# Kernel optimization log

Hardware: AMD Instinct MI355X
Metric: run time of the kernel (lower is better)

The kernel has to match this reference:

```python
import jax, jax.numpy as jnp
import numpy as np

_LAYER_SHAPES = ((10, 8), (8, 8), (8, 1))


def setup_inputs() -> dict:
    key = jax.random.key(0)
    k1, k2, k3, k4 = jax.random.split(key, 4)
    B, D, H, W = 8, 8, 256, 256
    M = 256
    E = jax.random.normal(k1, (B, D, H, W), dtype=jnp.float32)
    theta = jax.random.normal(k2, (M, 169), dtype=jnp.float32)
    centers = jax.random.uniform(k3, (M, 2), dtype=jnp.float32)
    batch_index = jax.random.randint(k4, (M,), 0, B)
    return {"E": E, "theta": theta, "centers": centers, "batch_index": batch_index}


def reference(E, theta, centers, batch_index):
    B, D, H, W = E.shape
    M = theta.shape[0]
    dt = E.dtype
    # pixel-center grid in [0,1]: linspace(0.5/H, 1-0.5/H, H)
    ys = (jnp.arange(H, dtype=dt) + 0.5) / H
    xs = (jnp.arange(W, dtype=dt) + 0.5) / W
    grid_y, grid_x = jnp.meshgrid(ys, xs, indexing="ij")
    grid = jnp.stack([grid_x, grid_y], axis=0)  # (2, H, W), channel order (x, y)
    rel = grid[None] - centers.astype(dt)[:, :, None, None]  # (M, 2, H, W)

    e_per_match = E[batch_index]  # (M, D, H, W) gather
    x = jnp.concatenate([e_per_match, rel], axis=1)  # (M, D+2, H, W)

    # split flat theta into per-layer 1x1 conv weights/biases and apply
    offset = 0
    n_layers = len(_LAYER_SHAPES)
    for li, (c_in, c_out) in enumerate(_LAYER_SHAPES):
        w = theta[:, offset:offset + c_in * c_out].reshape(M, c_out, c_in)
        offset += c_in * c_out
        b = theta[:, offset:offset + c_out]
        offset += c_out
        # per-instance 1x1 conv == tiny batched matmul over channels
        x = jnp.einsum("moi,mihw->mohw", w, x) + b[:, :, None, None]
        if li < n_layers - 1:
            x = jax.nn.gelu(x, approximate=False)  # torch F.gelu default (erf)
    return x[:, 0]  # (M, H, W) mask logits
```

## Files before the change

### kernel.cpp

```cpp
#include <hip/hip_runtime.h>
#include <math.h>

#define HWPIX 65536
#define NMATCH 256
#define THETA_LEN 169

__device__ __forceinline__ float gelu_fast(float v) {
    float t = fmaf(v * v, 0.10294323f, 2.3022082f);
    float e = __builtin_amdgcn_exp2f(-v * t);
    float r = __builtin_amdgcn_rcpf(1.0f + e);
    return v * r;
}

__global__ __launch_bounds__(256) void dmh_kernel(
    const float* __restrict__ E,
    const float* __restrict__ theta,
    const float* __restrict__ centers,
    const int*   __restrict__ bidx,
    float* __restrict__ out)
{
    const int m    = blockIdx.x >> 6;
    const int tile = blockIdx.x & 63;
    const int p0   = tile * 1024 + threadIdx.x * 4;

    const float* __restrict__ th = theta + m * THETA_LEN;
    const float cx = centers[2 * m];
    const float cy = centers[2 * m + 1];
    const int   b  = bidx[m];
    const float* __restrict__ Eb = E + (size_t)b * (8 * HWPIX) + p0;

    const int h = p0 >> 8;
    const int w = p0 & 255;

    float x[10][4];
    #pragma unroll
    for (int c = 0; c < 8; ++c) {
        const float4 v = *(const float4*)(Eb + (size_t)c * HWPIX);
        x[c][0] = v.x; x[c][1] = v.y; x[c][2] = v.z; x[c][3] = v.w;
    }
    #pragma unroll
    for (int j = 0; j < 4; ++j) {
        x[8][j] = (w + j + 0.5f) * (1.0f / 256.0f) - cx;
        x[9][j] = (h + 0.5f) * (1.0f / 256.0f) - cy;
    }

    float y[8][4];
    #pragma unroll
    for (int o = 0; o < 8; ++o) {
        const float bias = th[80 + o];
        float a[4] = {bias, bias, bias, bias};
        #pragma unroll
        for (int i = 0; i < 10; ++i) {
            const float wv = th[o * 10 + i];
            #pragma unroll
            for (int j = 0; j < 4; ++j) a[j] = fmaf(wv, x[i][j], a[j]);
        }
        #pragma unroll
        for (int j = 0; j < 4; ++j) y[o][j] = gelu_fast(a[j]);
    }

    float z[8][4];
    #pragma unroll
    for (int o = 0; o < 8; ++o) {
        const float bias = th[152 + o];
        float a[4] = {bias, bias, bias, bias};
        #pragma unroll
        for (int i = 0; i < 8; ++i) {
            const float wv = th[88 + o * 8 + i];
            #pragma unroll
            for (int j = 0; j < 4; ++j) a[j] = fmaf(wv, y[i][j], a[j]);
        }
        #pragma unroll
        for (int j = 0; j < 4; ++j) z[o][j] = gelu_fast(a[j]);
    }

    const float b2 = th[168];
    float r[4] = {b2, b2, b2, b2};
    #pragma unroll
    for (int i = 0; i < 8; ++i) {
        const float wv = th[160 + i];
        #pragma unroll
        for (int j = 0; j < 4; ++j) r[j] = fmaf(wv, z[i][j], r[j]);
    }

    float4 o4;
    o4.x = r[0]; o4.y = r[1]; o4.z = r[2]; o4.w = r[3];
    *(float4*)(out + (size_t)m * HWPIX + p0) = o4;
}

extern "C" void kernel_launch(void* const* d_in, const int* in_sizes, int n_in,
                              void* d_out, int out_size, void* d_ws, size_t ws_size,
                              hipStream_t stream) {
    const float* E       = (const float*)d_in[0];
    const float* theta   = (const float*)d_in[1];
    const float* centers = (const float*)d_in[2];
    const int*   bidx    = (const int*)d_in[3];
    float* out = (float*)d_out;

    dim3 grid(NMATCH * 64);
    dim3 block(256);
    hipLaunchKernelGGL(dmh_kernel, grid, block, 0, stream, E, theta, centers, bidx, out);
}
```

Before: 177.5 us.

## Use packed fp16 dot2 for per-instance MLP with pre-packed theta

Adds a small pre-pass kernel that packs the per-instance weights into fp16 pairs in workspace. The main kernel converts inputs and activations to packed half2 and uses v_dot2 with fp32 accumulation, roughly halving the FMA instruction count. This costs an extra kernel launch, conversion instructions and fp16 rounding of activations and weights, which may affect accuracy. The fp32 path is kept as a fallback when no workspace is available.

```diff
diff --git a/kernel.cpp b/kernel.cpp
--- a/kernel.cpp
+++ b/kernel.cpp
@@ -4,6 +4,10 @@
 #define HWPIX 65536
 #define NMATCH 256
 #define THETA_LEN 169
+#define TPK_STRIDE 128
+#define TPK_BYTES (NMATCH * TPK_STRIDE * 4)
+
+typedef __fp16 half2v __attribute__((ext_vector_type(2)));
 
 __device__ __forceinline__ float gelu_fast(float v) {
     float t = fmaf(v * v, 0.10294323f, 2.3022082f);
@@ -12,7 +16,143 @@
     return v * r;
 }
 
-__global__ __launch_bounds__(256) void dmh_kernel(
+__device__ __forceinline__ half2v as_h2(uint32_t u) {
+    union { uint32_t u; half2v h; } c; c.u = u; return c.h;
+}
+__device__ __forceinline__ float as_f32(uint32_t u) {
+    union { uint32_t u; float f; } c; c.u = u; return c.f;
+}
+
+__global__ __launch_bounds__(96) void pack_theta(
+    const float* __restrict__ theta, uint32_t* __restrict__ tpk)
+{
+    const int m = blockIdx.x;
+    const int t = threadIdx.x;
+    const float* __restrict__ th = theta + m * THETA_LEN;
+    uint32_t* __restrict__ o = tpk + m * TPK_STRIDE;
+
+    float a = 0.f, b = 0.f;
+    bool isPack = true;
+    if (t < 40) {
+        int oo = t / 5, k = t % 5;
+        if (k < 4) { a = th[oo * 10 + 2 * k]; b = th[oo * 10 + 2 * k + 1]; }
+        else       { a = th[oo * 10 + 8];     b = th[oo * 10 + 9]; }
+    } else if (t < 48) { isPack = false; a = th[80 + (t - 40)]; }
+    else if (t < 80) {
+        int oo = (t - 48) / 4, k = (t - 48) % 4;
+        a = th[88 + oo * 8 + 2 * k]; b = th[88 + oo * 8 + 2 * k + 1];
+    } else if (t < 88) { isPack = false; a = th[152 + (t - 80)]; }
+    else if (t < 92) { int k = t - 88; a = th[160 + 2 * k]; b = th[160 + 2 * k + 1]; }
+    else if (t == 92) { isPack = false; a = th[168]; }
+    else return;
+
+    uint32_t r;
+    if (isPack) {
+        half2v h = __builtin_amdgcn_cvt_pkrtz(a, b);
+        union { half2v h; uint32_t u; } c; c.h = h; r = c.u;
+    } else {
+        union { float f; uint32_t u; } c; c.f = a; r = c.u;
+    }
+    o[t] = r;
+}
+
+__global__ __launch_bounds__(256) void dmh_kernel_dot2(
+    const float* __restrict__ E,
+    const uint32_t* __restrict__ tpk,
+    const float* __restrict__ centers,
+    const int*   __restrict__ bidx,
+    float* __restrict__ out)
+{
+    const int m    = blockIdx.x >> 6;
+    const int tile = blockIdx.x & 63;
+    const int p0   = tile * 1024 + threadIdx.x * 4;
+
+    const uint32_t* __restrict__ tp = tpk + m * TPK_STRIDE;
+    const float cx = centers[2 * m];
+    const float cy = centers[2 * m + 1];
+    const int   b  = bidx[m];
+    const float* __restrict__ Eb = E + (size_t)b * (8 * HWPIX) + p0;
+
+    const int h = p0 >> 8;
+    const int w = p0 & 255;
+
+    half2v xp[5][4];
+    #pragma unroll
+    for (int cp = 0; cp < 4; ++cp) {
+        const float4 v0 = *(const float4*)(Eb + (size_t)(2 * cp) * HWPIX);
+        const float4 v1 = *(const float4*)(Eb + (size_t)(2 * cp + 1) * HWPIX);
+        xp[cp][0] = __builtin_amdgcn_cvt_pkrtz(v0.x, v1.x);
+        xp[cp][1] = __builtin_amdgcn_cvt_pkrtz(v0.y, v1.y);
+        xp[cp][2] = __builtin_amdgcn_cvt_pkrtz(v0.z, v1.z);
+        xp[cp][3] = __builtin_amdgcn_cvt_pkrtz(v0.w, v1.w);
+    }
+    const float ry = (h + 0.5f) * (1.0f / 256.0f) - cy;
+    #pragma unroll
+    for (int j = 0; j < 4; ++j) {
+        const float rx = (w + j + 0.5f) * (1.0f / 256.0f) - cx;
+        xp[4][j] = __builtin_amdgcn_cvt_pkrtz(rx, ry);
+    }
+
+    float yv[8][4];
+    #pragma unroll
+    for (int o = 0; o < 8; ++o) {
+        const float bias = as_f32(tp[40 + o]);
+        float a[4] = {bias, bias, bias, bias};
+        #pragma unroll
+        for (int k = 0; k < 5; ++k) {
+            const half2v wv = as_h2(tp[o * 5 + k]);
+            #pragma unroll
+            for (int j = 0; j < 4; ++j)
+                a[j] = __builtin_amdgcn_fdot2(wv, xp[k][j], a[j], false);
+        }
+        #pragma unroll
+        for (int j = 0; j < 4; ++j) yv[o][j] = gelu_fast(a[j]);
+    }
+    half2v yp[4][4];
+    #pragma unroll
+    for (int cp = 0; cp < 4; ++cp)
+        #pragma unroll
+        for (int j = 0; j < 4; ++j)
+            yp[cp][j] = __builtin_amdgcn_cvt_pkrtz(yv[2 * cp][j], yv[2 * cp + 1][j]);
+
+    float zv[8][4];
+    #pragma unroll
+    for (int o = 0; o < 8; ++o) {
+        const float bias = as_f32(tp[80 + o]);
+        float a[4] = {bias, bias, bias, bias};
+        #pragma unroll
+        for (int k = 0; k < 4; ++k) {
+            const half2v wv = as_h2(tp[48 + o * 4 + k]);
+            #pragma unroll
+            for (int j = 0; j < 4; ++j)
+                a[j] = __builtin_amdgcn_fdot2(wv, yp[k][j], a[j], false);
+        }
+        #pragma unroll
+        for (int j = 0; j < 4; ++j) zv[o][j] = gelu_fast(a[j]);
+    }
+    half2v zp[4][4];
+    #pragma unroll
+    for (int cp = 0; cp < 4; ++cp)
+        #pragma unroll
+        for (int j = 0; j < 4; ++j)
+            zp[cp][j] = __builtin_amdgcn_cvt_pkrtz(zv[2 * cp][j], zv[2 * cp + 1][j]);
+
+    const float b2 = as_f32(tp[92]);
+    float r[4] = {b2, b2, b2, b2};
+    #pragma unroll
+    for (int k = 0; k < 4; ++k) {
+        const half2v wv = as_h2(tp[88 + k]);
+        #pragma unroll
+        for (int j = 0; j < 4; ++j)
+            r[j] = __builtin_amdgcn_fdot2(wv, zp[k][j], r[j], false);
+    }
+
+    float4 o4;
+    o4.x = r[0]; o4.y = r[1]; o4.z = r[2]; o4.w = r[3];
+    *(float4*)(out + (size_t)m * HWPIX + p0) = o4;
+}
+
+__global__ __launch_bounds__(256) void dmh_kernel_f32(
     const float* __restrict__ E,
     const float* __restrict__ theta,
     const float* __restrict__ centers,
@@ -97,7 +237,14 @@
     const int*   bidx    = (const int*)d_in[3];
     float* out = (float*)d_out;
 
-    dim3 grid(NMATCH * 64);
-    dim3 block(256);
-    hipLaunchKernelGGL(dmh_kernel, grid, block, 0, stream, E, theta, centers, bidx, out);
-}
+    if (ws_size >= (size_t)TPK_BYTES && d_ws != nullptr) {
+        uint32_t* tpk = (uint32_t*)d_ws;
+        hipLaunchKernelGGL(pack_theta, dim3(NMATCH), dim3(96), 0, stream,
+                           theta, tpk);
+        hipLaunchKernelGGL(dmh_kernel_dot2, dim3(NMATCH * 64), dim3(256), 0, stream,
+                           E, tpk, centers, bidx, out);
+    } else {
+        hipLaunchKernelGGL(dmh_kernel_f32, dim3(NMATCH * 64), dim3(256), 0, stream,
+                           E, theta, centers, bidx, out);
+    }
+}
```

Result: slower. 188.5 us (+6.2%).

## Run the per-pixel MLP layers on fp16 MFMA 16x16x32 instructions

Applied to the files above, without the earlier changes.

Replaces the scalar FMA per-pixel MLP with three chained MFMA 16x16x32 f16 operations per step. Each wave handles 16 pixels per step over 128 steps, using bpermute shuffles to move the GELU outputs between layers. The weights are packed to fp16 and zero-padded into the A operand, with biases held in the accumulator. The intent is to offload the FMAs to the matrix cores. The cost is low MFMA utilization from padding, extra shuffles, duplicated scalar loads, narrow 16-float stores and reduced fp16 precision.

```diff
diff --git a/kernel.cpp b/kernel.cpp
--- a/kernel.cpp
+++ b/kernel.cpp
@@ -4,6 +4,12 @@
 #define HWPIX 65536
 #define NMATCH 256
 #define THETA_LEN 169
+
+typedef __fp16 h2   __attribute__((ext_vector_type(2)));
+typedef __fp16 h8   __attribute__((ext_vector_type(8)));
+typedef float  f32x4 __attribute__((ext_vector_type(4)));
+typedef unsigned int u32;
+typedef u32    u32x4 __attribute__((ext_vector_type(4)));
 
 __device__ __forceinline__ float gelu_fast(float v) {
     float t = fmaf(v * v, 0.10294323f, 2.3022082f);
@@ -12,80 +18,111 @@
     return v * r;
 }
 
-__global__ __launch_bounds__(256) void dmh_kernel(
+__device__ __forceinline__ u32 pkh(float a, float b) {
+    return __builtin_bit_cast(u32, __builtin_amdgcn_cvt_pkrtz(a, b));
+}
+__device__ __forceinline__ h8 mk8(u32 d0, u32 d1, u32 d2, u32 d3) {
+    u32x4 t; t[0] = d0; t[1] = d1; t[2] = d2; t[3] = d3;
+    return __builtin_bit_cast(h8, t);
+}
+__device__ __forceinline__ float bperm_f(int addr, float v) {
+    return __builtin_bit_cast(float,
+        __builtin_amdgcn_ds_bpermute(addr, __builtin_bit_cast(int, v)));
+}
+
+__global__ __launch_bounds__(256) void dmh_mfma(
     const float* __restrict__ E,
     const float* __restrict__ theta,
     const float* __restrict__ centers,
     const int*   __restrict__ bidx,
     float* __restrict__ out)
 {
-    const int m    = blockIdx.x >> 6;
-    const int tile = blockIdx.x & 63;
-    const int p0   = tile * 1024 + threadIdx.x * 4;
+    const int l     = threadIdx.x & 63;
+    const int gw    = blockIdx.x * 4 + (threadIdx.x >> 6);
+    const int m     = gw >> 5;
+    const int chunk = gw & 31;
 
     const float* __restrict__ th = theta + m * THETA_LEN;
     const float cx = centers[2 * m];
     const float cy = centers[2 * m + 1];
     const int   b  = bidx[m];
-    const float* __restrict__ Eb = E + (size_t)b * (8 * HWPIX) + p0;
+    const float* __restrict__ Eb = E + (size_t)b * (8 * HWPIX);
 
-    const int h = p0 >> 8;
-    const int w = p0 & 255;
+    const int mr = l & 15;
+    const int g  = l >> 4;
 
-    float x[10][4];
-    #pragma unroll
-    for (int c = 0; c < 8; ++c) {
-        const float4 v = *(const float4*)(Eb + (size_t)c * HWPIX);
-        x[c][0] = v.x; x[c][1] = v.y; x[c][2] = v.z; x[c][3] = v.w;
-    }
+    u32 a0[4], a1[4], a2[4];
     #pragma unroll
     for (int j = 0; j < 4; ++j) {
-        x[8][j] = (w + j + 0.5f) * (1.0f / 256.0f) - cx;
-        x[9][j] = (h + 0.5f) * (1.0f / 256.0f) - cy;
+        const int k0 = 8 * g + 2 * j;
+        const float w00 = (mr < 8 && k0     < 10) ? th[mr * 10 + k0]     : 0.f;
+        const float w01 = (mr < 8 && k0 + 1 < 10) ? th[mr * 10 + k0 + 1] : 0.f;
+        a0[j] = pkh(w00, w01);
+        const float w10 = (mr < 8 && g == 0) ? th[88 + mr * 8 + 2 * j]     : 0.f;
+        const float w11 = (mr < 8 && g == 0) ? th[88 + mr * 8 + 2 * j + 1] : 0.f;
+        a1[j] = pkh(w10, w11);
+        const float w20 = (mr == 0 && g == 0) ? th[160 + 2 * j]     : 0.f;
+        const float w21 = (mr == 0 && g == 0) ? th[160 + 2 * j + 1] : 0.f;
+        a2[j] = pkh(w20, w21);
+    }
+    const h8 A0 = mk8(a0[0], a0[1], a0[2], a0[3]);
+    const h8 A1 = mk8(a1[0], a1[1], a1[2], a1[3]);
+    const h8 A2 = mk8(a2[0], a2[1], a2[2], a2[3]);
+
+    f32x4 Cb0, Cb1, Cb2;
+    #pragma unroll
+    for (int r = 0; r < 4; ++r) {
+        const int row = 4 * g + r;
+        Cb0[r] = (row < 8) ? th[80 + row]  : 0.f;
+        Cb1[r] = (row < 8) ? th[152 + row] : 0.f;
+        Cb2[r] = (row == 0) ? th[168]      : 0.f;
     }
 
-    float y[8][4];
-    #pragma unroll
-    for (int o = 0; o < 8; ++o) {
-        const float bias = th[80 + o];
-        float a[4] = {bias, bias, bias, bias};
+    const int a0addr = 4 * mr;
+    const int a1addr = a0addr + 64;
+
+    int p = chunk * 2048 + mr;
+    float* __restrict__ outp = out + (size_t)m * HWPIX;
+
+    for (int step = 0; step < 128; ++step, p += 16) {
+        u32 b0[4];
         #pragma unroll
-        for (int i = 0; i < 10; ++i) {
-            const float wv = th[o * 10 + i];
-            #pragma unroll
-            for (int j = 0; j < 4; ++j) a[j] = fmaf(wv, x[i][j], a[j]);
+        for (int j = 0; j < 4; ++j)
+            b0[j] = pkh(Eb[(size_t)(2 * j) * HWPIX + p],
+                        Eb[(size_t)(2 * j + 1) * HWPIX + p]);
+        const int   wc = p & 255;
+        const int   hr = p >> 8;
+        const float rx = (wc + 0.5f) * (1.0f / 256.0f) - cx;
+        const float ry = (hr + 0.5f) * (1.0f / 256.0f) - cy;
+        const u32 rel = pkh(rx, ry);
+        if (g == 1) b0[0] = rel;
+        const f32x4 C0 = __builtin_amdgcn_mfma_f32_16x16x32_f16(
+            A0, mk8(b0[0], b0[1], b0[2], b0[3]), Cb0, 0, 0, 0);
+
+        float v[8];
+        #pragma unroll
+        for (int r = 0; r < 4; ++r) {
+            const float gv = gelu_fast(C0[r]);
+            v[r]     = bperm_f(a0addr, gv);
+            v[4 + r] = bperm_f(a1addr, gv);
         }
+        const f32x4 C1 = __builtin_amdgcn_mfma_f32_16x16x32_f16(
+            A1, mk8(pkh(v[0], v[1]), pkh(v[2], v[3]),
+                    pkh(v[4], v[5]), pkh(v[6], v[7])), Cb1, 0, 0, 0);
+
+        float u[8];
         #pragma unroll
-        for (int j = 0; j < 4; ++j) y[o][j] = gelu_fast(a[j]);
+        for (int r = 0; r < 4; ++r) {
+            const float gv = gelu_fast(C1[r]);
+            u[r]     = bperm_f(a0addr, gv);
+            u[4 + r] = bperm_f(a1addr, gv);
+        }
+        const f32x4 C2 = __builtin_amdgcn_mfma_f32_16x16x32_f16(
+            A2, mk8(pkh(u[0], u[1]), pkh(u[2], u[3]),
+                    pkh(u[4], u[5]), pkh(u[6], u[7])), Cb2, 0, 0, 0);
+
+        if (l < 16) outp[p] = C2[0];
     }
-
-    float z[8][4];
-    #pragma unroll
-    for (int o = 0; o < 8; ++o) {
-        const float bias = th[152 + o];
-        float a[4] = {bias, bias, bias, bias};
-        #pragma unroll
-        for (int i = 0; i < 8; ++i) {
-            const float wv = th[88 + o * 8 + i];
-            #pragma unroll
-            for (int j = 0; j < 4; ++j) a[j] = fmaf(wv, y[i][j], a[j]);
-        }
-        #pragma unroll
-        for (int j = 0; j < 4; ++j) z[o][j] = gelu_fast(a[j]);
-    }
-
-    const float b2 = th[168];
-    float r[4] = {b2, b2, b2, b2};
-    #pragma unroll
-    for (int i = 0; i < 8; ++i) {
-        const float wv = th[160 + i];
-        #pragma unroll
-        for (int j = 0; j < 4; ++j) r[j] = fmaf(wv, z[i][j], r[j]);
-    }
-
-    float4 o4;
-    o4.x = r[0]; o4.y = r[1]; o4.z = r[2]; o4.w = r[3];
-    *(float4*)(out + (size_t)m * HWPIX + p0) = o4;
 }
 
 extern "C" void kernel_launch(void* const* d_in, const int* in_sizes, int n_in,
@@ -97,7 +134,7 @@
     const int*   bidx    = (const int*)d_in[3];
     float* out = (float*)d_out;
 
-    dim3 grid(NMATCH * 64);
+    dim3 grid(NMATCH * 32 / 4);
     dim3 block(256);
-    hipLaunchKernelGGL(dmh_kernel, grid, block, 0, stream, E, theta, centers, bidx, out);
+    hipLaunchKernelGGL(dmh_mfma, grid, block, 0, stream, E, theta, centers, bidx, out);
 }
```

New measurement: 279.3 us. 57.3% more time.

## Replace GELU evaluation with shared-memory lookup table and linear interpolation

Applied to the files above, without the earlier changes.

Adds a small kernel that precomputes an exact-erf GELU table over [-8,8) at 1/64 spacing, stored as value and slope pairs, into workspace. The main kernel copies it into LDS and evaluates GELU by clamp, index and one FMA. Inputs, biases and the final weights are pre-scaled by 64 so table indices fall straight out of the accumulators. This swaps exp2 and rcp transcendental work for LDS gathers, which can cause bank conflicts. It also adds a per-block table copy and barrier, clamps inputs outside the table range, and uses piecewise-linear accuracy.

```diff
diff --git a/kernel.cpp b/kernel.cpp
--- a/kernel.cpp
+++ b/kernel.cpp
@@ -4,6 +4,119 @@
 #define HWPIX 65536
 #define NMATCH 256
 #define THETA_LEN 169
+#define TAB_N 1024
+#define TAB_BYTES (TAB_N * 8)
+
+__device__ __forceinline__ float gelu_exact(float x) {
+    return 0.5f * x * (1.0f + erff(x * 0.70710678118654752f));
+}
+
+__global__ __launch_bounds__(256) void fill_tab(float2* __restrict__ gtab) {
+    const int i = blockIdx.x * 256 + threadIdx.x;
+    if (i >= TAB_N) return;
+    const float x0 = (i - 512) * (1.0f / 64.0f);
+    const float x1 = (i - 511) * (1.0f / 64.0f);
+    const float g0 = 64.0f * gelu_exact(x0);
+    const float g1 = 64.0f * gelu_exact(x1);
+    float2 e; e.x = g0; e.y = g1 - g0;
+    gtab[i] = e;
+}
+
+__device__ __forceinline__ float gelu_lut(float xi, const float2* __restrict__ tab) {
+    const float xc = fminf(fmaxf(xi, 0.0f), 1023.0f);
+    const int   i  = (int)xc;
+    const float fr = xi - (float)i;
+    const float2 t = tab[i];
+    return fmaf(fr, t.y, t.x);
+}
+
+__global__ __launch_bounds__(256) void dmh_lut(
+    const float* __restrict__ E,
+    const float* __restrict__ theta,
+    const float* __restrict__ centers,
+    const int*   __restrict__ bidx,
+    const float2* __restrict__ gtab,
+    float* __restrict__ out)
+{
+    __shared__ float2 tab[TAB_N];
+    {
+        const float4* gt = (const float4*)gtab;
+        float4* st = (float4*)tab;
+        st[threadIdx.x]       = gt[threadIdx.x];
+        st[threadIdx.x + 256] = gt[threadIdx.x + 256];
+    }
+    __syncthreads();
+
+    const int m    = blockIdx.x >> 6;
+    const int tile = blockIdx.x & 63;
+    const int p0   = tile * 1024 + threadIdx.x * 4;
+
+    const float* __restrict__ th = theta + m * THETA_LEN;
+    const float cx64 = 64.0f * centers[2 * m];
+    const float cy64 = 64.0f * centers[2 * m + 1];
+    const int   b    = bidx[m];
+    const float* __restrict__ Eb = E + (size_t)b * (8 * HWPIX) + p0;
+
+    const int h = p0 >> 8;
+    const int w = p0 & 255;
+
+    float x[10][4];
+    #pragma unroll
+    for (int c = 0; c < 8; ++c) {
+        const float4 v = *(const float4*)(Eb + (size_t)c * HWPIX);
+        x[c][0] = v.x * 64.0f; x[c][1] = v.y * 64.0f;
+        x[c][2] = v.z * 64.0f; x[c][3] = v.w * 64.0f;
+    }
+    const float ry64 = (h + 0.5f) * 0.25f - cy64;
+    #pragma unroll
+    for (int j = 0; j < 4; ++j) {
+        x[8][j] = (w + j + 0.5f) * 0.25f - cx64;
+        x[9][j] = ry64;
+    }
+
+    float y[8][4];
+    #pragma unroll
+    for (int o = 0; o < 8; ++o) {
+        const float ainit = fmaf(th[80 + o], 64.0f, 512.0f);
+        float a[4] = {ainit, ainit, ainit, ainit};
+        #pragma unroll
+        for (int i = 0; i < 10; ++i) {
+            const float wv = th[o * 10 + i];
+            #pragma unroll
+            for (int j = 0; j < 4; ++j) a[j] = fmaf(wv, x[i][j], a[j]);
+        }
+        #pragma unroll
+        for (int j = 0; j < 4; ++j) y[o][j] = gelu_lut(a[j], tab);
+    }
+
+    float z[8][4];
+    #pragma unroll
+    for (int o = 0; o < 8; ++o) {
+        const float ainit = fmaf(th[152 + o], 64.0f, 512.0f);
+        float a[4] = {ainit, ainit, ainit, ainit};
+        #pragma unroll
+        for (int i = 0; i < 8; ++i) {
+            const float wv = th[88 + o * 8 + i];
+            #pragma unroll
+            for (int j = 0; j < 4; ++j) a[j] = fmaf(wv, y[i][j], a[j]);
+        }
+        #pragma unroll
+        for (int j = 0; j < 4; ++j) z[o][j] = gelu_lut(a[j], tab);
+    }
+
+    const float b2 = th[168];
+    float r[4] = {b2, b2, b2, b2};
+    #pragma unroll
+    for (int i = 0; i < 8; ++i) {
+        const float wv = th[160 + i] * (1.0f / 64.0f);
+        #pragma unroll
+        for (int j = 0; j < 4; ++j) r[j] = fmaf(wv, z[i][j], r[j]);
+    }
+
+    float4 o4;
+    o4.x = r[0]; o4.y = r[1]; o4.z = r[2]; o4.w = r[3];
+    *(float4*)(out + (size_t)m * HWPIX + p0) = o4;
+}
 
 __device__ __forceinline__ float gelu_fast(float v) {
     float t = fmaf(v * v, 0.10294323f, 2.3022082f);
@@ -12,7 +125,7 @@
     return v * r;
 }
 
-__global__ __launch_bounds__(256) void dmh_kernel(
+__global__ __launch_bounds__(256) void dmh_kernel_f32(
     const float* __restrict__ E,
     const float* __restrict__ theta,
     const float* __restrict__ centers,
@@ -97,7 +210,13 @@
     const int*   bidx    = (const int*)d_in[3];
     float* out = (float*)d_out;
 
-    dim3 grid(NMATCH * 64);
-    dim3 block(256);
-    hipLaunchKernelGGL(dmh_kernel, grid, block, 0, stream, E, theta, centers, bidx, out);
-}
+    if (ws_size >= (size_t)TAB_BYTES && d_ws != nullptr) {
+        float2* gtab = (float2*)d_ws;
+        hipLaunchKernelGGL(fill_tab, dim3(4), dim3(256), 0, stream, gtab);
+        hipLaunchKernelGGL(dmh_lut, dim3(NMATCH * 64), dim3(256), 0, stream,
+                           E, theta, centers, bidx, gtab, out);
+    } else {
+        hipLaunchKernelGGL(dmh_kernel_f32, dim3(NMATCH * 64), dim3(256), 0, stream,
+                           E, theta, centers, bidx, out);
+    }
+}
```

After: 171.0 us. 1.04x faster.
